# Optimization experiments

Hardware: AMD Instinct MI355X
Metric: run time of the kernel (lower is better)

Reference implementation:

```python
import jax, jax.numpy as jnp
import numpy as np

DIM = 768
HEADS = 12
HEAD_DIM = DIM // HEADS
HIDDEN = 4 * DIM
SCALE = HEAD_DIM ** -0.5
LN_EPS = 1e-5


def layer_norm(x, g, b):
    mu = jnp.mean(x, axis=-1, keepdims=True)
    var = jnp.var(x, axis=-1, keepdims=True)
    return (x - mu) * jax.lax.rsqrt(var + LN_EPS) * g + b


def setup_inputs() -> dict:
    key = jax.random.key(0)
    ks = jax.random.split(key, 10)
    B, N = 2, 2048
    s = 0.02
    return {
        "x": jax.random.normal(ks[0], (B, N, DIM), jnp.float32),
        "elevation": jax.random.uniform(ks[1], (B, N), jnp.float32),
        "qkv_w": jax.random.normal(ks[2], (DIM, 3 * DIM), jnp.float32) * s,
        "qkv_b": jnp.zeros((3 * DIM,), jnp.float32),
        "proj_w": jax.random.normal(ks[3], (DIM, DIM), jnp.float32) * s,
        "proj_b": jnp.zeros((DIM,), jnp.float32),
        "ln1_g": jnp.ones((DIM,), jnp.float32),
        "ln1_b": jnp.zeros((DIM,), jnp.float32),
        "ln2_g": jnp.ones((DIM,), jnp.float32),
        "ln2_b": jnp.zeros((DIM,), jnp.float32),
        "fc1_w": jax.random.normal(ks[4], (DIM, HIDDEN), jnp.float32) * s,
        "fc1_b": jnp.zeros((HIDDEN,), jnp.float32),
        "fc2_w": jax.random.normal(ks[5], (HIDDEN, DIM), jnp.float32) * s,
        "fc2_b": jnp.zeros((DIM,), jnp.float32),
        "barrier": jnp.asarray(3.0, jnp.float32),
    }


def reference(x, elevation, qkv_w, qkv_b, proj_w, proj_b, ln1_g, ln1_b,
              ln2_g, ln2_b, fc1_w, fc1_b, fc2_w, fc2_b, barrier):
    B, N, C = x.shape
    h = layer_norm(x, ln1_g, ln1_b)
    qkv = (h @ qkv_w + qkv_b).reshape(B, N, 3, HEADS, HEAD_DIM)
    q, k, v = jnp.moveaxis(qkv, 2, 0)  # each [B, N, H, D]
    # scores: [B, H, N, N]
    scores = jnp.einsum('bnhd,bmhd->bhnm', q, k) * SCALE
    w = jax.nn.softmax(scores, axis=-1)
    # pairwise elevation mask [B, N, N]: sigmoid(-s * (elev_j - elev_i))
    diff = elevation[:, None, :] - elevation[:, :, None]
    mask = jnp.clip(jax.nn.sigmoid(-barrier * diff), 1e-6, 1.0)
    w = w * mask[:, None, :, :]
    w = w / (jnp.sum(w, axis=-1, keepdims=True) + 1e-8)
    attn_out = jnp.einsum('bhnm,bmhd->bnhd', w, v).reshape(B, N, C)
    x = x + attn_out @ proj_w + proj_b
    h2 = layer_norm(x, ln2_g, ln2_b)
    mlp = jax.nn.gelu(h2 @ fc1_w + fc1_b, approximate=False) @ fc2_w + fc2_b
    return x + mlp
```

## Files before the change

kernel.cpp:

```cpp
#include <hip/hip_runtime.h>
#include <math.h>

#define DIM 768
#define HEADS 12
#define SEQ 2048
#define ROWS 4096
#define LN_EPS 1e-5f

typedef __attribute__((ext_vector_type(8))) short short8;
typedef __attribute__((ext_vector_type(4))) float floatx4;
typedef __attribute__((ext_vector_type(16))) float floatx16;
typedef unsigned short ushort_t;

__device__ __forceinline__ ushort_t f2bf(float x) {
    unsigned u = __float_as_uint(x);
    u += 0x7fff + ((u >> 16) & 1);
    return (ushort_t)(u >> 16);
}

__device__ __forceinline__ void gload_lds16(const void* g, void* l) {
    __builtin_amdgcn_global_load_lds((const __attribute__((address_space(1))) void*)g,
                                     (__attribute__((address_space(3))) void*)l, 16, 0, 0);
}

__launch_bounds__(256)
__global__ void wconv_all(const float* __restrict__ w0, const float* __restrict__ w1,
                          const float* __restrict__ w2, const float* __restrict__ w3,
                          ushort_t* __restrict__ t0, ushort_t* __restrict__ t1,
                          ushort_t* __restrict__ t2, ushort_t* __restrict__ t3) {
    __shared__ __align__(16) ushort_t s[64][72];
    int bid = blockIdx.x;
    const float* W; ushort_t* WT; int K, N, nx, id;
    if (bid < 432)       { W = w0; WT = t0; K = 768;  N = 2304; nx = 36; id = bid; }
    else if (bid < 576)  { W = w1; WT = t1; K = 768;  N = 768;  nx = 12; id = bid - 432; }
    else if (bid < 1152) { W = w2; WT = t2; K = 768;  N = 3072; nx = 48; id = bid - 576; }
    else                 { W = w3; WT = t3; K = 3072; N = 768;  nx = 12; id = bid - 1152; }
    int tx = id % nx, ty = id / nx;
    int k0 = ty * 64, n0 = tx * 64;
    int t = threadIdx.x;
    int rr0 = t >> 4, c4 = (t & 15) * 4;
    for (int rr = rr0; rr < 64; rr += 16) {
        float4 w = *(const float4*)(W + (size_t)(k0 + rr) * N + n0 + c4);
        s[c4 + 0][rr] = f2bf(w.x); s[c4 + 1][rr] = f2bf(w.y);
        s[c4 + 2][rr] = f2bf(w.z); s[c4 + 3][rr] = f2bf(w.w);
    }
    __syncthreads();
    int nl = t >> 2, kq = (t & 3) * 16;
    uint4 a = *(const uint4*)&s[nl][kq];
    uint4 b = *(const uint4*)&s[nl][kq + 8];
    *(uint4*)(WT + (size_t)(n0 + nl) * K + k0 + kq) = a;
    *(uint4*)(WT + (size_t)(n0 + nl) * K + k0 + kq + 8) = b;
}

__launch_bounds__(256)
__global__ void gelev_kernel(const float* __restrict__ elev, const float* __restrict__ barrier_p,
                             float* __restrict__ G, float* __restrict__ C2) {
    int i = blockIdx.x * 256 + threadIdx.x;
    float be = barrier_p[0] * elev[i];
    G[i]  = __expf(be);
    C2[i] = be;
}

__launch_bounds__(256)
__global__ void ln_kernel(const float* __restrict__ x, const float* __restrict__ g,
                          const float* __restrict__ b, ushort_t* __restrict__ out) {
    int row = blockIdx.x;
    const float* xr = x + (size_t)row * DIM;
    int t = threadIdx.x;
    float v0 = xr[t], v1 = xr[t + 256], v2 = xr[t + 512];
    float s  = v0 + v1 + v2;
    float ss = v0 * v0 + v1 * v1 + v2 * v2;
    #pragma unroll
    for (int o = 32; o >= 1; o >>= 1) { s += __shfl_xor(s, o); ss += __shfl_xor(ss, o); }
    __shared__ float rs[4], rss[4];
    int wid = t >> 6, lane = t & 63;
    if (lane == 0) { rs[wid] = s; rss[wid] = ss; }
    __syncthreads();
    if (t == 0) {
        float S = 0.f, SS = 0.f;
        for (int i = 0; i < 4; i++) { S += rs[i]; SS += rss[i]; }
        rs[0] = S; rss[0] = SS;
    }
    __syncthreads();
    float mean = rs[0] * (1.0f / DIM);
    float var  = rss[0] * (1.0f / DIM) - mean * mean;
    float rstd = rsqrtf(var + LN_EPS);
    ushort_t* orow = out + (size_t)row * DIM;
    orow[t]       = f2bf((v0 - mean) * rstd * g[t]       + b[t]);
    orow[t + 256] = f2bf((v1 - mean) * rstd * g[t + 256] + b[t + 256]);
    orow[t + 512] = f2bf((v2 - mean) * rstd * g[t + 512] + b[t + 512]);
}


#define G32_PREFETCH(K0, SA, SB)                                                      \
    {                                                                                 \
        int c0_ = t, r0_ = c0_ >> 2, bl0_ = c0_ & 3;                                  \
        gload_lds16(A  + (size_t)(row0 + r0_) * K + (K0) + ((bl0_ ^ (r0_ & 3)) << 3), &SA[c0_ * 8]); \
        gload_lds16(WT + (size_t)(col0 + r0_) * K + (K0) + ((bl0_ ^ (r0_ & 3)) << 3), &SB[c0_ * 8]); \
        int c1_ = 256 + t, r1_ = c1_ >> 2, bl1_ = c1_ & 3;                            \
        gload_lds16(A  + (size_t)(row0 + r1_) * K + (K0) + ((bl1_ ^ (r1_ & 3)) << 3), &SA[c1_ * 8]); \
        gload_lds16(WT + (size_t)(col0 + r1_) * K + (K0) + ((bl1_ ^ (r1_ & 3)) << 3), &SB[c1_ * 8]); \
    }

#define G32_COMPUTE(SA, SB)                                                           \
    {                                                                                 \
        _Pragma("unroll")                                                             \
        for (int s = 0; s < 2; s++) {                                                 \
            int blk_ = s * 2 + hb;                                                    \
            short8 a0_ = *(const short8*)&SA[ra0 * 32 + ((blk_ ^ (ra0 & 3)) << 3)];   \
            short8 a1_ = *(const short8*)&SA[ra1 * 32 + ((blk_ ^ (ra1 & 3)) << 3)];   \
            short8 b0_ = *(const short8*)&SB[rb0 * 32 + ((blk_ ^ (rb0 & 3)) << 3)];   \
            short8 b1_ = *(const short8*)&SB[rb1 * 32 + ((blk_ ^ (rb1 & 3)) << 3)];   \
            acc[0][0] = __builtin_amdgcn_mfma_f32_32x32x16_bf16(a0_, b0_, acc[0][0], 0, 0, 0); \
            acc[0][1] = __builtin_amdgcn_mfma_f32_32x32x16_bf16(a0_, b1_, acc[0][1], 0, 0, 0); \
            acc[1][0] = __builtin_amdgcn_mfma_f32_32x32x16_bf16(a1_, b0_, acc[1][0], 0, 0, 0); \
            acc[1][1] = __builtin_amdgcn_mfma_f32_32x32x16_bf16(a1_, b1_, acc[1][1], 0, 0, 0); \
        }                                                                             \
    }

template<int EPI>
__launch_bounds__(256)
__global__ void gemm32(const ushort_t* __restrict__ A, const ushort_t* __restrict__ WT,
                       const float* __restrict__ bias, ushort_t* __restrict__ outB,
                       ushort_t* __restrict__ qb, ushort_t* __restrict__ kb,
                       ushort_t* __restrict__ vb, int N, int K) {
    __shared__ __align__(16) ushort_t sA0[128 * 32];
    __shared__ __align__(16) ushort_t sA1[128 * 32];
    __shared__ __align__(16) ushort_t sB0[128 * 32];
    __shared__ __align__(16) ushort_t sB1[128 * 32];
    int t = threadIdx.x;
    int row0 = blockIdx.y * 128, col0 = blockIdx.x * 128;
    int wid = t >> 6, lane = t & 63, l31 = lane & 31, hb = lane >> 5;
    int wm = wid >> 1, wn = wid & 1;
    int ra0 = wm * 64 + l31, ra1 = ra0 + 32;
    int rb0 = wn * 64 + l31, rb1 = rb0 + 32;

    floatx16 acc[2][2];
    #pragma unroll
    for (int i = 0; i < 2; i++)
        #pragma unroll
        for (int j = 0; j < 2; j++)
            #pragma unroll
            for (int e = 0; e < 16; e++) acc[i][j][e] = 0.f;

    G32_PREFETCH(0, sA0, sB0)
    for (int k0 = 0; k0 < K; k0 += 64) {
        __syncthreads();
        if (k0 + 32 < K) G32_PREFETCH(k0 + 32, sA1, sB1)
        G32_COMPUTE(sA0, sB0)
        __syncthreads();
        if (k0 + 64 < K) G32_PREFETCH(k0 + 64, sA0, sB0)
        G32_COMPUTE(sA1, sB1)
    }

    #pragma unroll
    for (int mt = 0; mt < 2; mt++) {
        #pragma unroll
        for (int nt = 0; nt < 2; nt++) {
            int gcol = col0 + wn * 64 + nt * 32 + l31;
            float bv = bias[gcol];
            if (EPI == 0) {
                int which = gcol / 768;
                int hc = gcol - which * 768;
                int hh = hc >> 6, d = hc & 63;
                #pragma unroll
                for (int rg = 0; rg < 16; rg++) {
                    int grow = row0 + wm * 64 + mt * 32 + (rg & 3) + 8 * (rg >> 2) + 4 * hb;
                    float v = acc[mt][nt][rg] + bv;
                    int b_ = grow >> 11, n = grow & 2047;
                    size_t bhh = (size_t)(b_ * 12 + hh);
                    if (which == 0)      qb[(bhh * 2048 + n) * 64 + d] = f2bf(v * 0.125f);
                    else if (which == 1) kb[(bhh * 2048 + n) * 64 + d] = f2bf(v);
                    else                 vb[(bhh * 64 + d) * 2048 + n] = f2bf(v);
                }
            } else {
                #pragma unroll
                for (int rg = 0; rg < 16; rg++) {
                    int grow = row0 + wm * 64 + mt * 32 + (rg & 3) + 8 * (rg >> 2) + 4 * hb;
                    float v = acc[mt][nt][rg] + bv;
                    v = 0.5f * v * (1.f + erff(v * 0.70710678118654752f));
                    outB[(size_t)grow * N + gcol] = f2bf(v);
                }
            }
        }
    }
}


#define GB_PREFETCH(K0, SA, SB)                                                       \
    {                                                                                 \
        int r_ = t >> 2, sub_ = t & 3;                                                \
        gload_lds16(A  + (size_t)(row0 + r_) * K + (K0) + sub_ * 8, &SA[t * 8]);      \
        gload_lds16(WT + (size_t)(col0 + r_) * K + (K0) + sub_ * 8, &SB[t * 8]);      \
    }

#define GB_COMPUTE(SA, SB)                                                            \
    {                                                                                 \
        short8 a_[2], b_[2];                                                          \
        _Pragma("unroll")                                                             \
        for (int i = 0; i < 2; i++)                                                   \
            a_[i] = *(const short8*)&SA[(wm * 32 + i * 16 + cl) * 32 + quad * 8];     \
        _Pragma("unroll")                                                             \
        for (int j = 0; j < 2; j++)                                                   \
            b_[j] = *(const short8*)&SB[(wn * 32 + j * 16 + cl) * 32 + quad * 8];     \
        _Pragma("unroll")                                                             \
        for (int i = 0; i < 2; i++)                                                   \
            _Pragma("unroll")                                                         \
            for (int j = 0; j < 2; j++)                                               \
                acc[i][j] = __builtin_amdgcn_mfma_f32_16x16x32_bf16(a_[i], b_[j], acc[i][j], 0, 0, 0); \
    }

__launch_bounds__(256)
__global__ void gemm_bf16(const ushort_t* __restrict__ A, const ushort_t* __restrict__ WT,
                          const float* __restrict__ bias, const float* __restrict__ res,
                          float* __restrict__ outF, int N, int K) {
    __shared__ __align__(16) ushort_t sA0[64 * 32];
    __shared__ __align__(16) ushort_t sA1[64 * 32];
    __shared__ __align__(16) ushort_t sB0[64 * 32];
    __shared__ __align__(16) ushort_t sB1[64 * 32];
    int t = threadIdx.x;
    int row0 = blockIdx.y * 64, col0 = blockIdx.x * 64;
    int wid = t >> 6, lane = t & 63;
    int wm = wid >> 1, wn = wid & 1;
    int cl = lane & 15, quad = lane >> 4;

    floatx4 acc[2][2];
    #pragma unroll
    for (int i = 0; i < 2; i++)
        #pragma unroll
        for (int j = 0; j < 2; j++) { floatx4 z = {0.f, 0.f, 0.f, 0.f}; acc[i][j] = z; }

    GB_PREFETCH(0, sA0, sB0)
    for (int k0 = 0; k0 < K; k0 += 64) {
        __syncthreads();
        if (k0 + 32 < K) GB_PREFETCH(k0 + 32, sA1, sB1)
        GB_COMPUTE(sA0, sB0)
        __syncthreads();
        if (k0 + 64 < K) GB_PREFETCH(k0 + 64, sA0, sB0)
        GB_COMPUTE(sA1, sB1)
    }

    #pragma unroll
    for (int i = 0; i < 2; i++) {
        #pragma unroll
        for (int j = 0; j < 2; j++) {
            int gcol = col0 + wn * 32 + j * 16 + cl;
            float bv = bias[gcol];
            #pragma unroll
            for (int rg = 0; rg < 4; rg++) {
                int grow = row0 + wm * 32 + i * 16 + quad * 4 + rg;
                float v = acc[i][j][rg] + bv + res[(size_t)grow * N + gcol];
                outF[(size_t)grow * N + gcol] = v;
            }
        }
    }
}

#define PREFETCH(K0N, KSN, VTN)                                                   \
    {                                                                             \
        const ushort_t* kbase_ = kb + (bh * 2048 + (K0N)) * 64;                   \
        const ushort_t* vbase_ = vb + bh * 131072 + (K0N);                        \
        int c0_ = t, r0_ = c0_ >> 3, b0_ = c0_ & 7;                               \
        gload_lds16(kbase_ + (r0_ << 6) + ((b0_ ^ (r0_ & 7)) << 3), &KSN[c0_ * 8]); \
        gload_lds16(vbase_ + (size_t)r0_ * 2048 + ((b0_ ^ (r0_ & 7)) << 3), &VTN[c0_ * 8]); \
        int c1_ = 256 + t, r1_ = c1_ >> 3, b1_ = c1_ & 7;                         \
        gload_lds16(kbase_ + (r1_ << 6) + ((b1_ ^ (r1_ & 7)) << 3), &KSN[c1_ * 8]); \
        gload_lds16(vbase_ + (size_t)r1_ * 2048 + ((b1_ ^ (r1_ & 7)) << 3), &VTN[c1_ * 8]); \
    }

#define ATTN_TILE(KT, KSC, VTC, KSN, VTN)                                         \
    {                                                                             \
        __syncthreads();                                                          \
        if ((KT) < 31) PREFETCH(((KT) + 1) * 64, KSN, VTN)                        \
        float gjv_[4];                                                            \
        gjv_[0] = G[b * 2048 + (KT) * 64 + cl];                                   \
        gjv_[1] = G[b * 2048 + (KT) * 64 + 16 + cl];                              \
        gjv_[2] = G[b * 2048 + (KT) * 64 + 32 + cl];                              \
        gjv_[3] = G[b * 2048 + (KT) * 64 + 48 + cl];                              \
        floatx4 s_[4];                                                            \
        s_[0] = c2init; s_[1] = c2init; s_[2] = c2init; s_[3] = c2init;           \
        _Pragma("unroll")                                                         \
        for (int kh = 0; kh < 2; kh++) {                                          \
            short8 aq_ = *(const short8*)&Qs[((wid * 16 + cl) << 6) + (((kh * 4 + quad) ^ (cl & 7)) << 3)]; \
            _Pragma("unroll")                                                     \
            for (int nt = 0; nt < 4; nt++) {                                      \
                short8 bk_ = *(const short8*)&KSC[((nt * 16 + cl) << 6) + (((kh * 4 + quad) ^ (cl & 7)) << 3)]; \
                s_[nt] = __builtin_amdgcn_mfma_f32_16x16x32_bf16(aq_, bk_, s_[nt], 0, 0, 0); \
            }                                                                     \
        }                                                                         \
        _Pragma("unroll")                                                         \
        for (int rg = 0; rg < 4; rg++) {                                          \
            int prow_ = wid * 16 + quad * 4 + rg;                                 \
            int r8_ = prow_ & 7, pb_ = prow_ << 6, cs_ = cl & 7, ch_ = cl >> 3;   \
            _Pragma("unroll")                                                     \
            for (int nt = 0; nt < 4; nt++) {                                      \
                float tf_ = __expf(s_[nt][rg]);                                   \
                float p_  = tf_ * __builtin_amdgcn_rcpf(gi[rg] + gjv_[nt]);       \
                sem[rg] += p_;                                                    \
                Ps[pb_ + (((nt * 2 + ch_) ^ r8_) << 3) + cs_] = (ushort_t)(__float_as_uint(p_) >> 16); \
            }                                                                     \
        }                                                                         \
        _Pragma("unroll")                                                         \
        for (int kh = 0; kh < 2; kh++) {                                          \
            short8 ap_ = *(const short8*)&Ps[((wid * 16 + cl) << 6) + (((kh * 4 + quad) ^ (cl & 7)) << 3)]; \
            _Pragma("unroll")                                                     \
            for (int dt = 0; dt < 4; dt++) {                                      \
                short8 bv_ = *(const short8*)&VTC[((dt * 16 + cl) << 6) + (((kh * 4 + quad) ^ (cl & 7)) << 3)]; \
                o[dt] = __builtin_amdgcn_mfma_f32_16x16x32_bf16(ap_, bv_, o[dt], 0, 0, 0); \
            }                                                                     \
        }                                                                         \
    }

__launch_bounds__(256)
__global__ void attn_mfma(const ushort_t* __restrict__ qb, const ushort_t* __restrict__ kb,
                          const ushort_t* __restrict__ vb, const float* __restrict__ G,
                          const float* __restrict__ C2, ushort_t* __restrict__ attn) {
    __shared__ __align__(16) ushort_t Qs[4096];
    __shared__ __align__(16) ushort_t Ks0[4096];
    __shared__ __align__(16) ushort_t Ks1[4096];
    __shared__ __align__(16) ushort_t Vt0[4096];
    __shared__ __align__(16) ushort_t Vt1[4096];
    __shared__ __align__(16) ushort_t Ps[4096];
    int qt = blockIdx.x, h = blockIdx.y, b = blockIdx.z;
    int t = threadIdx.x, wid = t >> 6, lane = t & 63;
    int cl = lane & 15, quad = lane >> 4;
    int q0 = qt * 64;
    size_t bh = (size_t)(b * 12 + h);

    const ushort_t* qbase = qb + (bh * 2048 + q0) * 64;
    #pragma unroll
    for (int i = 0; i < 2; i++) {
        int c = i * 256 + t, row = c >> 3, blk = c & 7;
        gload_lds16(qbase + (row << 6) + ((blk ^ (row & 7)) << 3), &Qs[c * 8]);
    }
    int qrow4 = b * 2048 + q0 + wid * 16 + quad * 4;
    float4 g4  = *(const float4*)(G  + qrow4);
    float4 c24 = *(const float4*)(C2 + qrow4);
    float gi[4]  = {g4.x, g4.y, g4.z, g4.w};
    floatx4 c2init = {c24.x, c24.y, c24.z, c24.w};

    PREFETCH(0, Ks0, Vt0)

    floatx4 o[4];
    #pragma unroll
    for (int j = 0; j < 4; j++) { floatx4 z = {0.f, 0.f, 0.f, 0.f}; o[j] = z; }
    float sem[4] = {0.f, 0.f, 0.f, 0.f};

    for (int kt = 0; kt < 32; kt += 2) {
        ATTN_TILE(kt,     Ks0, Vt0, Ks1, Vt1)
        ATTN_TILE(kt + 1, Ks1, Vt1, Ks0, Vt0)
    }

    #pragma unroll
    for (int rg = 0; rg < 4; rg++) {
        float m = sem[rg];
        #pragma unroll
        for (int off = 1; off < 16; off <<= 1) m += __shfl_xor(m, off);
        float inv = __builtin_amdgcn_rcpf(m);
        int grow = b * 2048 + q0 + wid * 16 + quad * 4 + rg;
        #pragma unroll
        for (int dt = 0; dt < 4; dt++)
            attn[(size_t)grow * 768 + h * 64 + dt * 16 + cl] = f2bf(o[dt][rg] * inv);
    }
}

extern "C" void kernel_launch(void* const* d_in, const int* in_sizes, int n_in,
                              void* d_out, int out_size, void* d_ws, size_t ws_size,
                              hipStream_t stream) {
    const float* x      = (const float*)d_in[0];
    const float* elev   = (const float*)d_in[1];
    const float* qkv_w  = (const float*)d_in[2];
    const float* qkv_b  = (const float*)d_in[3];
    const float* proj_w = (const float*)d_in[4];
    const float* proj_b = (const float*)d_in[5];
    const float* ln1_g  = (const float*)d_in[6];
    const float* ln1_b  = (const float*)d_in[7];
    const float* ln2_g  = (const float*)d_in[8];
    const float* ln2_b  = (const float*)d_in[9];
    const float* fc1_w  = (const float*)d_in[10];
    const float* fc1_b  = (const float*)d_in[11];
    const float* fc2_w  = (const float*)d_in[12];
    const float* fc2_b  = (const float*)d_in[13];
    const float* barrier= (const float*)d_in[14];
    float* out = (float*)d_out;
    char* ws = (char*)d_ws;

    ushort_t* h    = (ushort_t*)(ws + 0);
    ushort_t* qb   = (ushort_t*)(ws + 6291456);
    ushort_t* kb   = (ushort_t*)(ws + 12582912);
    ushort_t* vb   = (ushort_t*)(ws + 18874368);
    ushort_t* f1   = (ushort_t*)(ws + 0);
    ushort_t* attn = (ushort_t*)(ws + 25165824);
    ushort_t* h2   = (ushort_t*)(ws + 31457280);
    float*    Gf   = (float*)(ws + 31457280);
    float*    C2f  = (float*)(ws + 31473664);
    ushort_t* qkvT = (ushort_t*)(ws + 37748736);
    ushort_t* projT= (ushort_t*)(ws + 41287680);
    ushort_t* fc1T = (ushort_t*)(ws + 42467328);
    ushort_t* fc2T = (ushort_t*)(ws + 47185920);

    wconv_all<<<1728, 256, 0, stream>>>(qkv_w, proj_w, fc1_w, fc2_w, qkvT, projT, fc1T, fc2T);
    gelev_kernel<<<16, 256, 0, stream>>>(elev, barrier, Gf, C2f);

    ln_kernel<<<ROWS, 256, 0, stream>>>(x, ln1_g, ln1_b, h);
    gemm32<0><<<dim3(2304 / 128, 32), 256, 0, stream>>>(
        h, qkvT, qkv_b, nullptr, qb, kb, vb, 2304, 768);
    attn_mfma<<<dim3(32, HEADS, 2), 256, 0, stream>>>(qb, kb, vb, Gf, C2f, attn);
    gemm_bf16<<<dim3(768 / 64, 64), 256, 0, stream>>>(
        attn, projT, proj_b, x, out, 768, 768);
    ln_kernel<<<ROWS, 256, 0, stream>>>(out, ln2_g, ln2_b, h2);
    gemm32<1><<<dim3(3072 / 128, 32), 256, 0, stream>>>(
        h2, fc1T, fc1_b, f1, nullptr, nullptr, nullptr, 3072, 768);
    gemm_bf16<<<dim3(768 / 64, 64), 256, 0, stream>>>(
        f1, fc2T, fc2_b, out, out, 768, 3072);
}
```

Measured before the change: 319.9 us.

## Merge prep kernels into one launch and switch GEMMs to 16x16x32 MFMA

Three small preprocessing kernels (weight bf16 transpose, elevation exp, first LayerNorm) are folded into a single launch dispatched by block index, removing two launch overheads. The 128x128 tiled GEMMs move from 32x32x16 MFMA tiles to a 4x4 grid of 16x16x32 MFMA tiles per wave, with a new LDS XOR swizzle to match the new read pattern. The epilogue now writes four rows per lane per tile, which changes store coalescing, and the register footprint of the accumulators stays the same.

```diff
diff --git a/kernel.cpp b/kernel.cpp
--- a/kernel.cpp
+++ b/kernel.cpp
@@ -24,41 +24,68 @@
 }
 
 __launch_bounds__(256)
-__global__ void wconv_all(const float* __restrict__ w0, const float* __restrict__ w1,
-                          const float* __restrict__ w2, const float* __restrict__ w3,
-                          ushort_t* __restrict__ t0, ushort_t* __restrict__ t1,
-                          ushort_t* __restrict__ t2, ushort_t* __restrict__ t3) {
+__global__ void prep_all(const float* __restrict__ w0, const float* __restrict__ w1,
+                         const float* __restrict__ w2, const float* __restrict__ w3,
+                         ushort_t* __restrict__ t0, ushort_t* __restrict__ t1,
+                         ushort_t* __restrict__ t2, ushort_t* __restrict__ t3,
+                         const float* __restrict__ elev, const float* __restrict__ barrier_p,
+                         float* __restrict__ G, float* __restrict__ C2,
+                         const float* __restrict__ x, const float* __restrict__ ln1_g,
+                         const float* __restrict__ ln1_b, ushort_t* __restrict__ h) {
     __shared__ __align__(16) ushort_t s[64][72];
     int bid = blockIdx.x;
-    const float* W; ushort_t* WT; int K, N, nx, id;
-    if (bid < 432)       { W = w0; WT = t0; K = 768;  N = 2304; nx = 36; id = bid; }
-    else if (bid < 576)  { W = w1; WT = t1; K = 768;  N = 768;  nx = 12; id = bid - 432; }
-    else if (bid < 1152) { W = w2; WT = t2; K = 768;  N = 3072; nx = 48; id = bid - 576; }
-    else                 { W = w3; WT = t3; K = 3072; N = 768;  nx = 12; id = bid - 1152; }
-    int tx = id % nx, ty = id / nx;
-    int k0 = ty * 64, n0 = tx * 64;
     int t = threadIdx.x;
-    int rr0 = t >> 4, c4 = (t & 15) * 4;
-    for (int rr = rr0; rr < 64; rr += 16) {
-        float4 w = *(const float4*)(W + (size_t)(k0 + rr) * N + n0 + c4);
-        s[c4 + 0][rr] = f2bf(w.x); s[c4 + 1][rr] = f2bf(w.y);
-        s[c4 + 2][rr] = f2bf(w.z); s[c4 + 3][rr] = f2bf(w.w);
-    }
-    __syncthreads();
-    int nl = t >> 2, kq = (t & 3) * 16;
-    uint4 a = *(const uint4*)&s[nl][kq];
-    uint4 b = *(const uint4*)&s[nl][kq + 8];
-    *(uint4*)(WT + (size_t)(n0 + nl) * K + k0 + kq) = a;
-    *(uint4*)(WT + (size_t)(n0 + nl) * K + k0 + kq + 8) = b;
-}
-
-__launch_bounds__(256)
-__global__ void gelev_kernel(const float* __restrict__ elev, const float* __restrict__ barrier_p,
-                             float* __restrict__ G, float* __restrict__ C2) {
-    int i = blockIdx.x * 256 + threadIdx.x;
-    float be = barrier_p[0] * elev[i];
-    G[i]  = __expf(be);
-    C2[i] = be;
+    if (bid < 1728) {
+        const float* W; ushort_t* WT; int K, N, nx, id;
+        if (bid < 432)       { W = w0; WT = t0; K = 768;  N = 2304; nx = 36; id = bid; }
+        else if (bid < 576)  { W = w1; WT = t1; K = 768;  N = 768;  nx = 12; id = bid - 432; }
+        else if (bid < 1152) { W = w2; WT = t2; K = 768;  N = 3072; nx = 48; id = bid - 576; }
+        else                 { W = w3; WT = t3; K = 3072; N = 768;  nx = 12; id = bid - 1152; }
+        int tx = id % nx, ty = id / nx;
+        int k0 = ty * 64, n0 = tx * 64;
+        int rr0 = t >> 4, c4 = (t & 15) * 4;
+        for (int rr = rr0; rr < 64; rr += 16) {
+            float4 w = *(const float4*)(W + (size_t)(k0 + rr) * N + n0 + c4);
+            s[c4 + 0][rr] = f2bf(w.x); s[c4 + 1][rr] = f2bf(w.y);
+            s[c4 + 2][rr] = f2bf(w.z); s[c4 + 3][rr] = f2bf(w.w);
+        }
+        __syncthreads();
+        int nl = t >> 2, kq = (t & 3) * 16;
+        uint4 a = *(const uint4*)&s[nl][kq];
+        uint4 b = *(const uint4*)&s[nl][kq + 8];
+        *(uint4*)(WT + (size_t)(n0 + nl) * K + k0 + kq) = a;
+        *(uint4*)(WT + (size_t)(n0 + nl) * K + k0 + kq + 8) = b;
+    } else if (bid < 1744) {
+        int i = (bid - 1728) * 256 + t;
+        float be = barrier_p[0] * elev[i];
+        G[i]  = __expf(be);
+        C2[i] = be;
+    } else {
+        int row = bid - 1744;
+        const float* xr = x + (size_t)row * DIM;
+        float v0 = xr[t], v1 = xr[t + 256], v2 = xr[t + 512];
+        float sm  = v0 + v1 + v2;
+        float ss = v0 * v0 + v1 * v1 + v2 * v2;
+        #pragma unroll
+        for (int o = 32; o >= 1; o >>= 1) { sm += __shfl_xor(sm, o); ss += __shfl_xor(ss, o); }
+        __shared__ float rs[4], rss[4];
+        int wid = t >> 6, lane = t & 63;
+        if (lane == 0) { rs[wid] = sm; rss[wid] = ss; }
+        __syncthreads();
+        if (t == 0) {
+            float S = 0.f, SS = 0.f;
+            for (int i2 = 0; i2 < 4; i2++) { S += rs[i2]; SS += rss[i2]; }
+            rs[0] = S; rss[0] = SS;
+        }
+        __syncthreads();
+        float mean = rs[0] * (1.0f / DIM);
+        float var  = rss[0] * (1.0f / DIM) - mean * mean;
+        float rstd = rsqrtf(var + LN_EPS);
+        ushort_t* orow = h + (size_t)row * DIM;
+        orow[t]       = f2bf((v0 - mean) * rstd * ln1_g[t]       + ln1_b[t]);
+        orow[t + 256] = f2bf((v1 - mean) * rstd * ln1_g[t + 256] + ln1_b[t + 256]);
+        orow[t + 512] = f2bf((v2 - mean) * rstd * ln1_g[t + 512] + ln1_b[t + 512]);
+    }
 }
 
 __launch_bounds__(256)
@@ -92,35 +119,41 @@
 }
 
 
-#define G32_PREFETCH(K0, SA, SB)                                                      \
+#define G16_PREFETCH(K0, SA, SB)                                                      \
     {                                                                                 \
         int c0_ = t, r0_ = c0_ >> 2, bl0_ = c0_ & 3;                                  \
-        gload_lds16(A  + (size_t)(row0 + r0_) * K + (K0) + ((bl0_ ^ (r0_ & 3)) << 3), &SA[c0_ * 8]); \
-        gload_lds16(WT + (size_t)(col0 + r0_) * K + (K0) + ((bl0_ ^ (r0_ & 3)) << 3), &SB[c0_ * 8]); \
+        int sw0_ = bl0_ ^ ((r0_ ^ (r0_ >> 2)) & 3);                                   \
+        gload_lds16(A  + (size_t)(row0 + r0_) * K + (K0) + (sw0_ << 3), &SA[c0_ * 8]); \
+        gload_lds16(WT + (size_t)(col0 + r0_) * K + (K0) + (sw0_ << 3), &SB[c0_ * 8]); \
         int c1_ = 256 + t, r1_ = c1_ >> 2, bl1_ = c1_ & 3;                            \
-        gload_lds16(A  + (size_t)(row0 + r1_) * K + (K0) + ((bl1_ ^ (r1_ & 3)) << 3), &SA[c1_ * 8]); \
-        gload_lds16(WT + (size_t)(col0 + r1_) * K + (K0) + ((bl1_ ^ (r1_ & 3)) << 3), &SB[c1_ * 8]); \
-    }
-
-#define G32_COMPUTE(SA, SB)                                                           \
+        int sw1_ = bl1_ ^ ((r1_ ^ (r1_ >> 2)) & 3);                                   \
+        gload_lds16(A  + (size_t)(row0 + r1_) * K + (K0) + (sw1_ << 3), &SA[c1_ * 8]); \
+        gload_lds16(WT + (size_t)(col0 + r1_) * K + (K0) + (sw1_ << 3), &SB[c1_ * 8]); \
+    }
+
+#define G16_COMPUTE(SA, SB)                                                           \
     {                                                                                 \
-        _Pragma("unroll")                                                             \
-        for (int s = 0; s < 2; s++) {                                                 \
-            int blk_ = s * 2 + hb;                                                    \
-            short8 a0_ = *(const short8*)&SA[ra0 * 32 + ((blk_ ^ (ra0 & 3)) << 3)];   \
-            short8 a1_ = *(const short8*)&SA[ra1 * 32 + ((blk_ ^ (ra1 & 3)) << 3)];   \
-            short8 b0_ = *(const short8*)&SB[rb0 * 32 + ((blk_ ^ (rb0 & 3)) << 3)];   \
-            short8 b1_ = *(const short8*)&SB[rb1 * 32 + ((blk_ ^ (rb1 & 3)) << 3)];   \
-            acc[0][0] = __builtin_amdgcn_mfma_f32_32x32x16_bf16(a0_, b0_, acc[0][0], 0, 0, 0); \
-            acc[0][1] = __builtin_amdgcn_mfma_f32_32x32x16_bf16(a0_, b1_, acc[0][1], 0, 0, 0); \
-            acc[1][0] = __builtin_amdgcn_mfma_f32_32x32x16_bf16(a1_, b0_, acc[1][0], 0, 0, 0); \
-            acc[1][1] = __builtin_amdgcn_mfma_f32_32x32x16_bf16(a1_, b1_, acc[1][1], 0, 0, 0); \
+        short8 a_[4], b_[4];                                                          \
+        _Pragma("unroll")                                                             \
+        for (int i = 0; i < 4; i++) {                                                 \
+            int ra_ = wm * 64 + i * 16 + cl;                                          \
+            a_[i] = *(const short8*)&SA[ra_ * 32 + ((quad ^ ((ra_ ^ (ra_ >> 2)) & 3)) << 3)]; \
         }                                                                             \
+        _Pragma("unroll")                                                             \
+        for (int j = 0; j < 4; j++) {                                                 \
+            int rb_ = wn * 64 + j * 16 + cl;                                          \
+            b_[j] = *(const short8*)&SB[rb_ * 32 + ((quad ^ ((rb_ ^ (rb_ >> 2)) & 3)) << 3)]; \
+        }                                                                             \
+        _Pragma("unroll")                                                             \
+        for (int i = 0; i < 4; i++)                                                   \
+            _Pragma("unroll")                                                         \
+            for (int j = 0; j < 4; j++)                                               \
+                acc[i][j] = __builtin_amdgcn_mfma_f32_16x16x32_bf16(a_[i], b_[j], acc[i][j], 0, 0, 0); \
     }
 
 template<int EPI>
 __launch_bounds__(256)
-__global__ void gemm32(const ushort_t* __restrict__ A, const ushort_t* __restrict__ WT,
+__global__ void gemm16(const ushort_t* __restrict__ A, const ushort_t* __restrict__ WT,
                        const float* __restrict__ bias, ushort_t* __restrict__ outB,
                        ushort_t* __restrict__ qb, ushort_t* __restrict__ kb,
                        ushort_t* __restrict__ vb, int N, int K) {
@@ -130,54 +163,46 @@
     __shared__ __align__(16) ushort_t sB1[128 * 32];
     int t = threadIdx.x;
     int row0 = blockIdx.y * 128, col0 = blockIdx.x * 128;
-    int wid = t >> 6, lane = t & 63, l31 = lane & 31, hb = lane >> 5;
+    int wid = t >> 6, lane = t & 63;
     int wm = wid >> 1, wn = wid & 1;
-    int ra0 = wm * 64 + l31, ra1 = ra0 + 32;
-    int rb0 = wn * 64 + l31, rb1 = rb0 + 32;
-
-    floatx16 acc[2][2];
-    #pragma unroll
-    for (int i = 0; i < 2; i++)
-        #pragma unroll
-        for (int j = 0; j < 2; j++)
+    int cl = lane & 15, quad = lane >> 4;
+
+    floatx4 acc[4][4];
+    #pragma unroll
+    for (int i = 0; i < 4; i++)
+        #pragma unroll
+        for (int j = 0; j < 4; j++) { floatx4 z = {0.f, 0.f, 0.f, 0.f}; acc[i][j] = z; }
+
+    G16_PREFETCH(0, sA0, sB0)
+    for (int k0 = 0; k0 < K; k0 += 64) {
+        __syncthreads();
+        if (k0 + 32 < K) G16_PREFETCH(k0 + 32, sA1, sB1)
+        G16_COMPUTE(sA0, sB0)
+        __syncthreads();
+        if (k0 + 64 < K) G16_PREFETCH(k0 + 64, sA0, sB0)
+        G16_COMPUTE(sA1, sB1)
+    }
+
+    #pragma unroll
+    for (int i = 0; i < 4; i++) {
+        #pragma unroll
+        for (int j = 0; j < 4; j++) {
+            int gcol = col0 + wn * 64 + j * 16 + cl;
+            float bv = bias[gcol];
             #pragma unroll
-            for (int e = 0; e < 16; e++) acc[i][j][e] = 0.f;
-
-    G32_PREFETCH(0, sA0, sB0)
-    for (int k0 = 0; k0 < K; k0 += 64) {
-        __syncthreads();
-        if (k0 + 32 < K) G32_PREFETCH(k0 + 32, sA1, sB1)
-        G32_COMPUTE(sA0, sB0)
-        __syncthreads();
-        if (k0 + 64 < K) G32_PREFETCH(k0 + 64, sA0, sB0)
-        G32_COMPUTE(sA1, sB1)
-    }
-
-    #pragma unroll
-    for (int mt = 0; mt < 2; mt++) {
-        #pragma unroll
-        for (int nt = 0; nt < 2; nt++) {
-            int gcol = col0 + wn * 64 + nt * 32 + l31;
-            float bv = bias[gcol];
-            if (EPI == 0) {
-                int which = gcol / 768;
-                int hc = gcol - which * 768;
-                int hh = hc >> 6, d = hc & 63;
-                #pragma unroll
-                for (int rg = 0; rg < 16; rg++) {
-                    int grow = row0 + wm * 64 + mt * 32 + (rg & 3) + 8 * (rg >> 2) + 4 * hb;
-                    float v = acc[mt][nt][rg] + bv;
+            for (int rg = 0; rg < 4; rg++) {
+                int grow = row0 + wm * 64 + i * 16 + quad * 4 + rg;
+                float v = acc[i][j][rg] + bv;
+                if (EPI == 0) {
+                    int which = gcol / 768;
+                    int hc = gcol - which * 768;
+                    int hh = hc >> 6, d = hc & 63;
                     int b_ = grow >> 11, n = grow & 2047;
                     size_t bhh = (size_t)(b_ * 12 + hh);
                     if (which == 0)      qb[(bhh * 2048 + n) * 64 + d] = f2bf(v * 0.125f);
                     else if (which == 1) kb[(bhh * 2048 + n) * 64 + d] = f2bf(v);
                     else                 vb[(bhh * 64 + d) * 2048 + n] = f2bf(v);
-                }
-            } else {
-                #pragma unroll
-                for (int rg = 0; rg < 16; rg++) {
-                    int grow = row0 + wm * 64 + mt * 32 + (rg & 3) + 8 * (rg >> 2) + 4 * hb;
-                    float v = acc[mt][nt][rg] + bv;
+                } else {
                     v = 0.5f * v * (1.f + erff(v * 0.70710678118654752f));
                     outB[(size_t)grow * N + gcol] = f2bf(v);
                 }
@@ -185,7 +210,6 @@
         }
     }
 }
-
 
 #define GB_PREFETCH(K0, SA, SB)                                                       \
     {                                                                                 \
@@ -399,17 +423,15 @@
     ushort_t* fc1T = (ushort_t*)(ws + 42467328);
     ushort_t* fc2T = (ushort_t*)(ws + 47185920);
 
-    wconv_all<<<1728, 256, 0, stream>>>(qkv_w, proj_w, fc1_w, fc2_w, qkvT, projT, fc1T, fc2T);
-    gelev_kernel<<<16, 256, 0, stream>>>(elev, barrier, Gf, C2f);
-
-    ln_kernel<<<ROWS, 256, 0, stream>>>(x, ln1_g, ln1_b, h);
-    gemm32<0><<<dim3(2304 / 128, 32), 256, 0, stream>>>(
+    prep_all<<<5840, 256, 0, stream>>>(qkv_w, proj_w, fc1_w, fc2_w, qkvT, projT, fc1T, fc2T,
+                                       elev, barrier, Gf, C2f, x, ln1_g, ln1_b, h);
+    gemm16<0><<<dim3(2304 / 128, 32), 256, 0, stream>>>(
         h, qkvT, qkv_b, nullptr, qb, kb, vb, 2304, 768);
     attn_mfma<<<dim3(32, HEADS, 2), 256, 0, stream>>>(qb, kb, vb, Gf, C2f, attn);
     gemm_bf16<<<dim3(768 / 64, 64), 256, 0, stream>>>(
         attn, projT, proj_b, x, out, 768, 768);
     ln_kernel<<<ROWS, 256, 0, stream>>>(out, ln2_g, ln2_b, h2);
-    gemm32<1><<<dim3(3072 / 128, 32), 256, 0, stream>>>(
+    gemm16<1><<<dim3(3072 / 128, 32), 256, 0, stream>>>(
         h2, fc1T, fc1_b, f1, nullptr, nullptr, nullptr, 3072, 768);
     gemm_bf16<<<dim3(768 / 64, 64), 256, 0, stream>>>(
         f1, fc2T, fc2_b, out, out, 768, 3072);
```

After: 312.8 us. 1.02x faster.
